# Optimization experiments

Hardware: AMD Instinct MI355X
Metric: run time of the kernel (lower is better)

## Reference

```python
import jax, jax.numpy as jnp
import numpy as np

OH, OW = 32, 32          # adaptive pool output size
NUM_KERNELS = 2
LATENT = 100             # latent_dims = [100, 100]
S = (OH // 2) * (OW // 2)  # in_spatial = 256


def adaptive_avg_pool(x, oh, ow):
    # exact-divisor adaptive avg pool == block mean
    B, C, H, W = x.shape
    return x.reshape(B, C, oh, H // oh, ow, W // ow).mean(axis=(3, 5))


def setup_inputs() -> dict:
    key = jax.random.key(0)
    k1, k2, k3, k4 = jax.random.split(key, 4)
    x = jax.random.normal(k1, (8, 512, 128, 128), dtype=jnp.float32)
    scale = 1.0 / np.sqrt(S)
    psi_w = jax.random.normal(k2, (NUM_KERNELS, S, LATENT), dtype=jnp.float32) * scale  # visible->latent proj
    phi_w = jax.random.normal(k3, (NUM_KERNELS, S, LATENT), dtype=jnp.float32) * scale  # latent->visible proj
    out_w = jax.random.normal(k4, (S, S), dtype=jnp.float32) * scale                    # output linear over spatial feats
    return {"x": x, "psi_w": psi_w, "phi_w": phi_w, "out_w": out_w}


def reference(x, psi_w, phi_w, out_w):
    B, C, H, W = x.shape
    # GAP: adaptive average pool to (OH, OW)
    xg = adaptive_avg_pool(x, OH, OW)                                   # [B,C,32,32]
    # internal 2x2 avg pool (accounts for in_spatial = h/2 * ceil(w/2))
    v = xg.reshape(B, C, OH // 2, 2, OW // 2, 2).mean(axis=(3, 5))
    v = v.reshape(B, C, S)                                              # channel nodes [B,C,S]
    # visible -> latent affinity (softmax over visible/channel nodes)
    A_v2l = jax.nn.softmax(jnp.einsum('bcs,ksd->bkdc', v, psi_w), axis=-1)  # [B,K,d1,C]
    z = jnp.einsum('bkdc,bcs->bkds', A_v2l, v).reshape(B, NUM_KERNELS * LATENT, S)  # [B,Kd1,S]
    # latent -> latent propagation on normalized features
    zn = z / (jnp.linalg.norm(z, axis=-1, keepdims=True) + 1e-6)
    G = jax.nn.softmax(jnp.einsum('bms,bns->bmn', zn, zn), axis=-1)     # [B,Kd1,Kd1]
    zp = jnp.einsum('bmn,bns->bms', G, z).reshape(B, NUM_KERNELS, LATENT, S)
    # latent -> visible affinity (softmax over latent nodes)
    A_l2v = jax.nn.softmax(jnp.einsum('bcs,ksd->bkcd', v, phi_w), axis=-1)  # [B,K,C,d2]
    out = jnp.einsum('bkcd,bkds->bcs', A_l2v, zp)                       # [B,C,S]
    out = jnp.einsum('bcs,st->bct', out, out_w)
    f = v + out                                                          # residual
    attn = jax.nn.sigmoid(f.mean(axis=-1))                               # [B,C]
    return attn[:, :, None, None]                                        # [B,C,1,1]
```

## Files before the change

kernel.cpp:

```cpp
#include <hip/hip_runtime.h>
#include <math.h>

constexpr int Bn = 8, Cn = 512, Sn = 256, Mn = 200, Ln = 100;

constexpr size_t OFF_V    = 0;
constexpr size_t OFF_A    = OFF_V   + (size_t)Bn*Cn*Sn;
constexpr size_t OFF_Z    = OFF_A   + (size_t)Bn*Mn*Cn;
constexpr size_t OFF_INV  = OFF_Z   + (size_t)Bn*Mn*Sn;
constexpr size_t OFF_ZW   = OFF_INV + (size_t)Bn*Mn;
constexpr size_t OFF_ZPW  = OFF_ZW  + (size_t)Bn*Mn;
constexpr size_t OFF_WSUM = OFF_ZPW + (size_t)Bn*Mn;

__device__ __forceinline__ float blk_max(float x, float* red) {
  #pragma unroll
  for (int o = 32; o; o >>= 1) x = fmaxf(x, __shfl_xor(x, o));
  __syncthreads();
  if ((threadIdx.x & 63) == 0) red[threadIdx.x >> 6] = x;
  __syncthreads();
  return fmaxf(fmaxf(red[0], red[1]), fmaxf(red[2], red[3]));
}
__device__ __forceinline__ float blk_sum(float x, float* red) {
  #pragma unroll
  for (int o = 32; o; o >>= 1) x += __shfl_xor(x, o);
  __syncthreads();
  if ((threadIdx.x & 63) == 0) red[threadIdx.x >> 6] = x;
  __syncthreads();
  return red[0] + red[1] + red[2] + red[3];
}

__global__ void k_wsum(const float* __restrict__ w, float* __restrict__ ws) {
  int t = threadIdx.x;
  const float* row = w + (size_t)t * Sn;
  float s = 0.f;
  for (int j = 0; j < Sn; j += 4) {
    float4 f = *(const float4*)(row + j);
    s += f.x + f.y + f.z + f.w;
  }
  ws[OFF_WSUM + t] = s;
}

__global__ void __launch_bounds__(256) k_pool(const float* __restrict__ x,
                                              float* __restrict__ ws) {
  int bc = blockIdx.x;
  const float* plane = x + (size_t)bc * 16384;
  int t = threadIdx.x;
  float part[16];
  #pragma unroll
  for (int i = 0; i < 16; ++i) {
    float4 f = *(const float4*)(plane + i * 1024 + t * 4);
    part[i] = f.x + f.y + f.z + f.w;
  }
  __shared__ float lds[256][17];
  #pragma unroll
  for (int i = 0; i < 16; ++i) lds[t][i] = part[i];
  __syncthreads();
  int i = t >> 4, jj = t & 15;
  float s = 0.f;
  #pragma unroll
  for (int r = 0; r < 8; ++r)
    s += lds[32 * r + 2 * jj][i] + lds[32 * r + 2 * jj + 1][i];
  ws[OFF_V + (size_t)bc * 256 + t] = s * (1.0f / 64.0f);
}

__global__ void __launch_bounds__(256) k_psm(const float* __restrict__ psi,
                                             float* __restrict__ ws) {
  int b = blockIdx.y, g = blockIdx.x, t = threadIdx.x;
  int m0 = g * 8;
  __shared__ float pc[8][256];
  __shared__ float red[4];
  const float* v = ws + OFF_V + (size_t)b * Cn * Sn;
  #pragma unroll
  for (int mm = 0; mm < 8; ++mm) {
    int m = m0 + mm, k = m / Ln, d = m % Ln;
    pc[mm][t] = psi[(size_t)k * Sn * Ln + (size_t)t * Ln + d];
  }
  __syncthreads();
  float acc[2][8];
  #pragma unroll
  for (int ci = 0; ci < 2; ++ci) {
    const float* vp = v + (size_t)(t + ci * 256) * Sn;
    float a[8] = {0, 0, 0, 0, 0, 0, 0, 0};
    for (int s = 0; s < Sn; s += 4) {
      float4 vv = *(const float4*)(vp + s);
      #pragma unroll
      for (int mm = 0; mm < 8; ++mm)
        a[mm] += vv.x * pc[mm][s] + vv.y * pc[mm][s + 1] +
                 vv.z * pc[mm][s + 2] + vv.w * pc[mm][s + 3];
    }
    #pragma unroll
    for (int mm = 0; mm < 8; ++mm) acc[ci][mm] = a[mm];
  }
  #pragma unroll
  for (int mm = 0; mm < 8; ++mm) {
    float mx = blk_max(fmaxf(acc[0][mm], acc[1][mm]), red);
    float e0 = expf(acc[0][mm] - mx), e1 = expf(acc[1][mm] - mx);
    float inv = 1.0f / blk_sum(e0 + e1, red);
    float* Arow = ws + OFF_A + ((size_t)b * Mn + m0 + mm) * Cn;
    Arow[t] = e0 * inv;
    Arow[t + 256] = e1 * inv;
  }
}

__global__ void __launch_bounds__(256) k_z(float* __restrict__ ws) {
  int b = blockIdx.y, g = blockIdx.x, t = threadIdx.x;
  int m0 = g * 8;
  __shared__ float As[8][512];
  __shared__ float red[4];
  const float* v = ws + OFF_V + (size_t)b * Cn * Sn;
  const float* A = ws + OFF_A + (size_t)b * Mn * Cn;
  #pragma unroll
  for (int mm = 0; mm < 8; ++mm) {
    As[mm][t]       = A[(size_t)(m0 + mm) * Cn + t];
    As[mm][t + 256] = A[(size_t)(m0 + mm) * Cn + t + 256];
  }
  __syncthreads();
  float acc[8] = {0, 0, 0, 0, 0, 0, 0, 0};
  for (int c = 0; c < Cn; ++c) {
    float vv = v[(size_t)c * Sn + t];
    #pragma unroll
    for (int mm = 0; mm < 8; ++mm) acc[mm] += As[mm][c] * vv;
  }
  float wsv = ws[OFF_WSUM + t];
  #pragma unroll
  for (int mm = 0; mm < 8; ++mm) {
    int m = m0 + mm;
    ws[OFF_Z + ((size_t)b * Mn + m) * Sn + t] = acc[mm];
    float n2 = blk_sum(acc[mm] * acc[mm], red);
    float zw = blk_sum(acc[mm] * wsv, red);
    if (t == 0) {
      ws[OFF_INV + (size_t)b * Mn + m] = 1.0f / (sqrtf(n2) + 1e-6f);
      ws[OFF_ZW  + (size_t)b * Mn + m] = zw;
    }
  }
}

__global__ void __launch_bounds__(256) k_g(float* __restrict__ ws) {
  int b = blockIdx.y, g = blockIdx.x, t = threadIdx.x;
  int m0 = g * 8;
  __shared__ float zl[8][256];
  __shared__ float invl[200], zwl[200];
  __shared__ float red[4];
  const float* z = ws + OFF_Z + (size_t)b * Mn * Sn;
  #pragma unroll
  for (int mm = 0; mm < 8; ++mm) zl[mm][t] = z[(size_t)(m0 + mm) * Sn + t];
  if (t < Mn) {
    invl[t] = ws[OFF_INV + (size_t)b * Mn + t];
    zwl[t]  = ws[OFF_ZW  + (size_t)b * Mn + t];
  }
  __syncthreads();
  float dot[8] = {0, 0, 0, 0, 0, 0, 0, 0};
  if (t < Mn) {
    const float* zr = z + (size_t)t * Sn;
    for (int s = 0; s < Sn; s += 4) {
      float4 zz = *(const float4*)(zr + s);
      #pragma unroll
      for (int mm = 0; mm < 8; ++mm)
        dot[mm] += zz.x * zl[mm][s] + zz.y * zl[mm][s + 1] +
                   zz.z * zl[mm][s + 2] + zz.w * zl[mm][s + 3];
    }
  }
  #pragma unroll
  for (int mm = 0; mm < 8; ++mm) {
    int m = m0 + mm;
    float val = (t < Mn) ? dot[mm] * invl[m] * invl[t] : -1e30f;
    float mx = blk_max(val, red);
    float e  = (t < Mn) ? expf(val - mx) : 0.f;
    float se  = blk_sum(e, red);
    float sez = blk_sum(e * ((t < Mn) ? zwl[t] : 0.f), red);
    if (t == 0) ws[OFF_ZPW + (size_t)b * Mn + m] = sez / se;
  }
}

__global__ void __launch_bounds__(256) k_out(const float* __restrict__ phi,
                                             float* __restrict__ out,
                                             float* __restrict__ ws) {
  int b = blockIdx.y, cg = blockIdx.x, t = threadIdx.x;
  int c0 = cg * 8;
  __shared__ float vl[8][256];
  __shared__ float zpl[200];
  __shared__ float t2l[16][104];
  __shared__ float resl[2][8];
  __shared__ float vsl[8];
  const float* v = ws + OFF_V + ((size_t)b * Cn + c0) * Sn;
  #pragma unroll
  for (int cc = 0; cc < 8; ++cc) vl[cc][t] = v[(size_t)cc * Sn + t];
  if (t < Mn) zpl[t] = ws[OFF_ZPW + (size_t)b * Mn + t];
  __syncthreads();
  int k = t >> 7, d = t & 127;
  int dd = d < Ln ? d : Ln - 1;
  const float* pp = phi + (size_t)k * Sn * Ln + dd;
  float acc[8] = {0, 0, 0, 0, 0, 0, 0, 0};
  for (int s = 0; s < Sn; ++s) {
    float p = pp[(size_t)s * Ln];
    #pragma unroll
    for (int cc = 0; cc < 8; ++cc) acc[cc] += vl[cc][s] * p;
  }
  if (d < Ln) {
    #pragma unroll
    for (int cc = 0; cc < 8; ++cc) t2l[k * 8 + cc][d] = acc[cc];
  }
  __syncthreads();
  int gg = t >> 4, l = t & 15;
  int k2 = gg >> 3, cc2 = gg & 7;
  float mx = -1e30f;
  for (int dq = l; dq < Ln; dq += 16) mx = fmaxf(mx, t2l[gg][dq]);
  #pragma unroll
  for (int o = 8; o; o >>= 1) mx = fmaxf(mx, __shfl_xor(mx, o));
  float se = 0.f, sez = 0.f;
  for (int dq = l; dq < Ln; dq += 16) {
    float e = expf(t2l[gg][dq] - mx);
    se += e;
    sez += e * zpl[k2 * Ln + dq];
  }
  #pragma unroll
  for (int o = 8; o; o >>= 1) { se += __shfl_xor(se, o); sez += __shfl_xor(sez, o); }
  float vs = 0.f;
  if (k2 == 0) {
    for (int i2 = 0; i2 < 16; ++i2) vs += vl[cc2][i2 * 16 + l];
    #pragma unroll
    for (int o = 8; o; o >>= 1) vs += __shfl_xor(vs, o);
    if (l == 0) vsl[cc2] = vs;
  }
  if (l == 0) resl[k2][cc2] = sez / se;
  __syncthreads();
  if (t < 8) {
    float f = (vsl[t] + resl[0][t] + resl[1][t]) * (1.0f / 256.0f);
    out[(size_t)b * Cn + c0 + t] = 1.0f / (1.0f + expf(-f));
  }
}

extern "C" void kernel_launch(void* const* d_in, const int* in_sizes, int n_in,
                              void* d_out, int out_size, void* d_ws, size_t ws_size,
                              hipStream_t stream) {
  const float* x   = (const float*)d_in[0];
  const float* psi = (const float*)d_in[1];
  const float* phi = (const float*)d_in[2];
  const float* ow  = (const float*)d_in[3];
  float* out = (float*)d_out;
  float* ws  = (float*)d_ws;

  hipLaunchKernelGGL(k_wsum, dim3(1),       dim3(256), 0, stream, ow, ws);
  hipLaunchKernelGGL(k_pool, dim3(4096),    dim3(256), 0, stream, x, ws);
  hipLaunchKernelGGL(k_psm,  dim3(25, 8),   dim3(256), 0, stream, psi, ws);
  hipLaunchKernelGGL(k_z,    dim3(25, 8),   dim3(256), 0, stream, ws);
  hipLaunchKernelGGL(k_g,    dim3(25, 8),   dim3(256), 0, stream, ws);
  hipLaunchKernelGGL(k_out,  dim3(64, 8),   dim3(256), 0, stream, phi, out, ws);
}
```

Before: 156.8 us.

## Fuse softmax-affinity and z kernels, fold wsum into pool, batch block reductions

Merges the psi softmax kernel and the z projection kernel into one 512-thread kernel that keeps the affinity matrix in LDS instead of writing and re-reading it through global memory. Folds the out_w row-sum into an extra block of the pool kernel, which removes a launch. Block reductions now handle four values at once to cut barrier count. k_g is split into 4-row groups to double its grid, and the inner loops use float4 LDS reads. The cost is higher LDS use per block and fewer, larger blocks in the fused kernel.

```diff
diff --git a/kernel.cpp b/kernel.cpp
--- a/kernel.cpp
+++ b/kernel.cpp
@@ -4,46 +4,66 @@
 constexpr int Bn = 8, Cn = 512, Sn = 256, Mn = 200, Ln = 100;
 
 constexpr size_t OFF_V    = 0;
-constexpr size_t OFF_A    = OFF_V   + (size_t)Bn*Cn*Sn;
-constexpr size_t OFF_Z    = OFF_A   + (size_t)Bn*Mn*Cn;
+constexpr size_t OFF_Z    = OFF_V   + (size_t)Bn*Cn*Sn;
 constexpr size_t OFF_INV  = OFF_Z   + (size_t)Bn*Mn*Sn;
 constexpr size_t OFF_ZW   = OFF_INV + (size_t)Bn*Mn;
 constexpr size_t OFF_ZPW  = OFF_ZW  + (size_t)Bn*Mn;
 constexpr size_t OFF_WSUM = OFF_ZPW + (size_t)Bn*Mn;
 
-__device__ __forceinline__ float blk_max(float x, float* red) {
-  #pragma unroll
-  for (int o = 32; o; o >>= 1) x = fmaxf(x, __shfl_xor(x, o));
+template<int NW>
+__device__ __forceinline__ float4 blk_max_f4(float4 x, float4* red) {
+  #pragma unroll
+  for (int o = 32; o; o >>= 1) {
+    x.x = fmaxf(x.x, __shfl_xor(x.x, o));
+    x.y = fmaxf(x.y, __shfl_xor(x.y, o));
+    x.z = fmaxf(x.z, __shfl_xor(x.z, o));
+    x.w = fmaxf(x.w, __shfl_xor(x.w, o));
+  }
   __syncthreads();
   if ((threadIdx.x & 63) == 0) red[threadIdx.x >> 6] = x;
   __syncthreads();
-  return fmaxf(fmaxf(red[0], red[1]), fmaxf(red[2], red[3]));
-}
-__device__ __forceinline__ float blk_sum(float x, float* red) {
-  #pragma unroll
-  for (int o = 32; o; o >>= 1) x += __shfl_xor(x, o);
+  float4 r = red[0];
+  #pragma unroll
+  for (int w = 1; w < NW; ++w) {
+    r.x = fmaxf(r.x, red[w].x); r.y = fmaxf(r.y, red[w].y);
+    r.z = fmaxf(r.z, red[w].z); r.w = fmaxf(r.w, red[w].w);
+  }
+  return r;
+}
+template<int NW>
+__device__ __forceinline__ float4 blk_sum_f4(float4 x, float4* red) {
+  #pragma unroll
+  for (int o = 32; o; o >>= 1) {
+    x.x += __shfl_xor(x.x, o); x.y += __shfl_xor(x.y, o);
+    x.z += __shfl_xor(x.z, o); x.w += __shfl_xor(x.w, o);
+  }
   __syncthreads();
   if ((threadIdx.x & 63) == 0) red[threadIdx.x >> 6] = x;
   __syncthreads();
-  return red[0] + red[1] + red[2] + red[3];
-}
-
-__global__ void k_wsum(const float* __restrict__ w, float* __restrict__ ws) {
+  float4 r = red[0];
+  #pragma unroll
+  for (int w = 1; w < NW; ++w) {
+    r.x += red[w].x; r.y += red[w].y; r.z += red[w].z; r.w += red[w].w;
+  }
+  return r;
+}
+
+__global__ void __launch_bounds__(256) k_pool(const float* __restrict__ x,
+                                              const float* __restrict__ ow,
+                                              float* __restrict__ ws) {
   int t = threadIdx.x;
-  const float* row = w + (size_t)t * Sn;
-  float s = 0.f;
-  for (int j = 0; j < Sn; j += 4) {
-    float4 f = *(const float4*)(row + j);
-    s += f.x + f.y + f.z + f.w;
-  }
-  ws[OFF_WSUM + t] = s;
-}
-
-__global__ void __launch_bounds__(256) k_pool(const float* __restrict__ x,
-                                              float* __restrict__ ws) {
+  if (blockIdx.x == 4096) {
+    const float* row = ow + (size_t)t * Sn;
+    float s = 0.f;
+    for (int j = 0; j < Sn; j += 4) {
+      float4 f = *(const float4*)(row + j);
+      s += f.x + f.y + f.z + f.w;
+    }
+    ws[OFF_WSUM + t] = s;
+    return;
+  }
   int bc = blockIdx.x;
   const float* plane = x + (size_t)bc * 16384;
-  int t = threadIdx.x;
   float part[16];
   #pragma unroll
   for (int i = 0; i < 16; ++i) {
@@ -62,112 +82,142 @@
   ws[OFF_V + (size_t)bc * 256 + t] = s * (1.0f / 64.0f);
 }
 
-__global__ void __launch_bounds__(256) k_psm(const float* __restrict__ psi,
+__global__ void __launch_bounds__(512) k_psz(const float* __restrict__ psi,
                                              float* __restrict__ ws) {
   int b = blockIdx.y, g = blockIdx.x, t = threadIdx.x;
   int m0 = g * 8;
-  __shared__ float pc[8][256];
-  __shared__ float red[4];
+  __shared__ __align__(16) float pc[8][256];
+  __shared__ __align__(16) float As[8][512];
+  __shared__ __align__(16) float zpart[2][8][256];
+  __shared__ float4 red4[8];
   const float* v = ws + OFF_V + (size_t)b * Cn * Sn;
-  #pragma unroll
-  for (int mm = 0; mm < 8; ++mm) {
+
+  for (int e = t; e < 8 * 256; e += 512) {
+    int mm = e >> 8, s = e & 255;
     int m = m0 + mm, k = m / Ln, d = m % Ln;
-    pc[mm][t] = psi[(size_t)k * Sn * Ln + (size_t)t * Ln + d];
-  }
-  __syncthreads();
-  float acc[2][8];
-  #pragma unroll
-  for (int ci = 0; ci < 2; ++ci) {
-    const float* vp = v + (size_t)(t + ci * 256) * Sn;
-    float a[8] = {0, 0, 0, 0, 0, 0, 0, 0};
+    pc[mm][s] = psi[(size_t)k * Sn * Ln + (size_t)s * Ln + d];
+  }
+  __syncthreads();
+
+  float acc[8] = {0, 0, 0, 0, 0, 0, 0, 0};
+  {
+    const float* vp = v + (size_t)t * Sn;
     for (int s = 0; s < Sn; s += 4) {
       float4 vv = *(const float4*)(vp + s);
       #pragma unroll
-      for (int mm = 0; mm < 8; ++mm)
-        a[mm] += vv.x * pc[mm][s] + vv.y * pc[mm][s + 1] +
-                 vv.z * pc[mm][s + 2] + vv.w * pc[mm][s + 3];
-    }
-    #pragma unroll
-    for (int mm = 0; mm < 8; ++mm) acc[ci][mm] = a[mm];
-  }
-  #pragma unroll
-  for (int mm = 0; mm < 8; ++mm) {
-    float mx = blk_max(fmaxf(acc[0][mm], acc[1][mm]), red);
-    float e0 = expf(acc[0][mm] - mx), e1 = expf(acc[1][mm] - mx);
-    float inv = 1.0f / blk_sum(e0 + e1, red);
-    float* Arow = ws + OFF_A + ((size_t)b * Mn + m0 + mm) * Cn;
-    Arow[t] = e0 * inv;
-    Arow[t + 256] = e1 * inv;
-  }
-}
-
-__global__ void __launch_bounds__(256) k_z(float* __restrict__ ws) {
-  int b = blockIdx.y, g = blockIdx.x, t = threadIdx.x;
-  int m0 = g * 8;
-  __shared__ float As[8][512];
-  __shared__ float red[4];
-  const float* v = ws + OFF_V + (size_t)b * Cn * Sn;
-  const float* A = ws + OFF_A + (size_t)b * Mn * Cn;
-  #pragma unroll
-  for (int mm = 0; mm < 8; ++mm) {
-    As[mm][t]       = A[(size_t)(m0 + mm) * Cn + t];
-    As[mm][t + 256] = A[(size_t)(m0 + mm) * Cn + t + 256];
-  }
-  __syncthreads();
-  float acc[8] = {0, 0, 0, 0, 0, 0, 0, 0};
-  for (int c = 0; c < Cn; ++c) {
-    float vv = v[(size_t)c * Sn + t];
-    #pragma unroll
-    for (int mm = 0; mm < 8; ++mm) acc[mm] += As[mm][c] * vv;
-  }
-  float wsv = ws[OFF_WSUM + t];
-  #pragma unroll
-  for (int mm = 0; mm < 8; ++mm) {
-    int m = m0 + mm;
-    ws[OFF_Z + ((size_t)b * Mn + m) * Sn + t] = acc[mm];
-    float n2 = blk_sum(acc[mm] * acc[mm], red);
-    float zw = blk_sum(acc[mm] * wsv, red);
+      for (int mm = 0; mm < 8; ++mm) {
+        float4 p = *(const float4*)&pc[mm][s];
+        acc[mm] += vv.x * p.x + vv.y * p.y + vv.z * p.z + vv.w * p.w;
+      }
+    }
+  }
+  #pragma unroll
+  for (int q = 0; q < 2; ++q) {
+    float4 a = make_float4(acc[4*q], acc[4*q+1], acc[4*q+2], acc[4*q+3]);
+    float4 mx = blk_max_f4<8>(a, red4);
+    float4 e;
+    e.x = expf(a.x - mx.x); e.y = expf(a.y - mx.y);
+    e.z = expf(a.z - mx.z); e.w = expf(a.w - mx.w);
+    float4 se = blk_sum_f4<8>(e, red4);
+    As[4*q+0][t] = e.x / se.x;
+    As[4*q+1][t] = e.y / se.y;
+    As[4*q+2][t] = e.z / se.z;
+    As[4*q+3][t] = e.w / se.w;
+  }
+  __syncthreads();
+
+  int h = t >> 8, s2 = t & 255;
+  float a2[8] = {0, 0, 0, 0, 0, 0, 0, 0};
+  const float* vb = v + (size_t)h * 256 * Sn;
+  for (int c = 0; c < 256; c += 4) {
+    float v0 = vb[(size_t)(c + 0) * Sn + s2];
+    float v1 = vb[(size_t)(c + 1) * Sn + s2];
+    float v2 = vb[(size_t)(c + 2) * Sn + s2];
+    float v3 = vb[(size_t)(c + 3) * Sn + s2];
+    #pragma unroll
+    for (int mm = 0; mm < 8; ++mm) {
+      float4 aa = *(const float4*)&As[mm][h * 256 + c];
+      a2[mm] += aa.x * v0 + aa.y * v1 + aa.z * v2 + aa.w * v3;
+    }
+  }
+  #pragma unroll
+  for (int mm = 0; mm < 8; ++mm) zpart[h][mm][s2] = a2[mm];
+  __syncthreads();
+
+  float zv[8] = {0, 0, 0, 0, 0, 0, 0, 0};
+  float wsv = 0.f;
+  if (t < 256) {
+    wsv = ws[OFF_WSUM + t];
+    float* zo = ws + OFF_Z + ((size_t)b * Mn + m0) * Sn;
+    #pragma unroll
+    for (int mm = 0; mm < 8; ++mm) {
+      zv[mm] = zpart[0][mm][t] + zpart[1][mm][t];
+      zo[(size_t)mm * Sn + t] = zv[mm];
+    }
+  }
+  #pragma unroll
+  for (int q = 0; q < 2; ++q) {
+    float4 sq = make_float4(zv[4*q]*zv[4*q], zv[4*q+1]*zv[4*q+1],
+                            zv[4*q+2]*zv[4*q+2], zv[4*q+3]*zv[4*q+3]);
+    float4 n2 = blk_sum_f4<8>(sq, red4);
+    float4 zw = blk_sum_f4<8>(make_float4(zv[4*q]*wsv, zv[4*q+1]*wsv,
+                                          zv[4*q+2]*wsv, zv[4*q+3]*wsv), red4);
     if (t == 0) {
-      ws[OFF_INV + (size_t)b * Mn + m] = 1.0f / (sqrtf(n2) + 1e-6f);
-      ws[OFF_ZW  + (size_t)b * Mn + m] = zw;
+      float* inv = ws + OFF_INV + (size_t)b * Mn + m0 + 4*q;
+      float* zwp = ws + OFF_ZW  + (size_t)b * Mn + m0 + 4*q;
+      inv[0] = 1.0f / (sqrtf(n2.x) + 1e-6f); zwp[0] = zw.x;
+      inv[1] = 1.0f / (sqrtf(n2.y) + 1e-6f); zwp[1] = zw.y;
+      inv[2] = 1.0f / (sqrtf(n2.z) + 1e-6f); zwp[2] = zw.z;
+      inv[3] = 1.0f / (sqrtf(n2.w) + 1e-6f); zwp[3] = zw.w;
     }
   }
 }
 
 __global__ void __launch_bounds__(256) k_g(float* __restrict__ ws) {
   int b = blockIdx.y, g = blockIdx.x, t = threadIdx.x;
-  int m0 = g * 8;
-  __shared__ float zl[8][256];
+  int m0 = g * 4;
+  __shared__ __align__(16) float zl[4][256];
   __shared__ float invl[200], zwl[200];
-  __shared__ float red[4];
+  __shared__ float4 red4[4];
   const float* z = ws + OFF_Z + (size_t)b * Mn * Sn;
   #pragma unroll
-  for (int mm = 0; mm < 8; ++mm) zl[mm][t] = z[(size_t)(m0 + mm) * Sn + t];
+  for (int mm = 0; mm < 4; ++mm) zl[mm][t] = z[(size_t)(m0 + mm) * Sn + t];
   if (t < Mn) {
     invl[t] = ws[OFF_INV + (size_t)b * Mn + t];
     zwl[t]  = ws[OFF_ZW  + (size_t)b * Mn + t];
   }
   __syncthreads();
-  float dot[8] = {0, 0, 0, 0, 0, 0, 0, 0};
-  if (t < Mn) {
+  bool act = t < Mn;
+  float dot[4] = {0, 0, 0, 0};
+  if (act) {
     const float* zr = z + (size_t)t * Sn;
     for (int s = 0; s < Sn; s += 4) {
       float4 zz = *(const float4*)(zr + s);
       #pragma unroll
-      for (int mm = 0; mm < 8; ++mm)
-        dot[mm] += zz.x * zl[mm][s] + zz.y * zl[mm][s + 1] +
-                   zz.z * zl[mm][s + 2] + zz.w * zl[mm][s + 3];
-    }
-  }
-  #pragma unroll
-  for (int mm = 0; mm < 8; ++mm) {
-    int m = m0 + mm;
-    float val = (t < Mn) ? dot[mm] * invl[m] * invl[t] : -1e30f;
-    float mx = blk_max(val, red);
-    float e  = (t < Mn) ? expf(val - mx) : 0.f;
-    float se  = blk_sum(e, red);
-    float sez = blk_sum(e * ((t < Mn) ? zwl[t] : 0.f), red);
-    if (t == 0) ws[OFF_ZPW + (size_t)b * Mn + m] = sez / se;
+      for (int mm = 0; mm < 4; ++mm) {
+        float4 zl4 = *(const float4*)&zl[mm][s];
+        dot[mm] += zz.x * zl4.x + zz.y * zl4.y + zz.z * zl4.z + zz.w * zl4.w;
+      }
+    }
+  }
+  float4 val;
+  val.x = act ? dot[0] * invl[m0 + 0] * invl[t] : -1e30f;
+  val.y = act ? dot[1] * invl[m0 + 1] * invl[t] : -1e30f;
+  val.z = act ? dot[2] * invl[m0 + 2] * invl[t] : -1e30f;
+  val.w = act ? dot[3] * invl[m0 + 3] * invl[t] : -1e30f;
+  float4 mx = blk_max_f4<4>(val, red4);
+  float4 e;
+  e.x = act ? expf(val.x - mx.x) : 0.f;
+  e.y = act ? expf(val.y - mx.y) : 0.f;
+  e.z = act ? expf(val.z - mx.z) : 0.f;
+  e.w = act ? expf(val.w - mx.w) : 0.f;
+  float4 se = blk_sum_f4<4>(e, red4);
+  float zwn = act ? zwl[t] : 0.f;
+  float4 sez = blk_sum_f4<4>(make_float4(e.x*zwn, e.y*zwn, e.z*zwn, e.w*zwn), red4);
+  if (t == 0) {
+    float* zp = ws + OFF_ZPW + (size_t)b * Mn + m0;
+    zp[0] = sez.x / se.x; zp[1] = sez.y / se.y;
+    zp[2] = sez.z / se.z; zp[3] = sez.w / se.w;
   }
 }
 
@@ -176,7 +226,7 @@
                                              float* __restrict__ ws) {
   int b = blockIdx.y, cg = blockIdx.x, t = threadIdx.x;
   int c0 = cg * 8;
-  __shared__ float vl[8][256];
+  __shared__ __align__(16) float vl[8][256];
   __shared__ float zpl[200];
   __shared__ float t2l[16][104];
   __shared__ float resl[2][8];
@@ -190,10 +240,16 @@
   int dd = d < Ln ? d : Ln - 1;
   const float* pp = phi + (size_t)k * Sn * Ln + dd;
   float acc[8] = {0, 0, 0, 0, 0, 0, 0, 0};
-  for (int s = 0; s < Sn; ++s) {
-    float p = pp[(size_t)s * Ln];
-    #pragma unroll
-    for (int cc = 0; cc < 8; ++cc) acc[cc] += vl[cc][s] * p;
+  for (int s = 0; s < Sn; s += 4) {
+    float p0 = pp[(size_t)(s + 0) * Ln];
+    float p1 = pp[(size_t)(s + 1) * Ln];
+    float p2 = pp[(size_t)(s + 2) * Ln];
+    float p3 = pp[(size_t)(s + 3) * Ln];
+    #pragma unroll
+    for (int cc = 0; cc < 8; ++cc) {
+      float4 vv = *(const float4*)&vl[cc][s];
+      acc[cc] += vv.x * p0 + vv.y * p1 + vv.z * p2 + vv.w * p3;
+    }
   }
   if (d < Ln) {
     #pragma unroll
@@ -239,10 +295,8 @@
   float* out = (float*)d_out;
   float* ws  = (float*)d_ws;
 
-  hipLaunchKernelGGL(k_wsum, dim3(1),       dim3(256), 0, stream, ow, ws);
-  hipLaunchKernelGGL(k_pool, dim3(4096),    dim3(256), 0, stream, x, ws);
-  hipLaunchKernelGGL(k_psm,  dim3(25, 8),   dim3(256), 0, stream, psi, ws);
-  hipLaunchKernelGGL(k_z,    dim3(25, 8),   dim3(256), 0, stream, ws);
-  hipLaunchKernelGGL(k_g,    dim3(25, 8),   dim3(256), 0, stream, ws);
-  hipLaunchKernelGGL(k_out,  dim3(64, 8),   dim3(256), 0, stream, phi, out, ws);
-}
+  hipLaunchKernelGGL(k_pool, dim3(4097),   dim3(256), 0, stream, x, ow, ws);
+  hipLaunchKernelGGL(k_psz,  dim3(25, 8),  dim3(512), 0, stream, psi, ws);
+  hipLaunchKernelGGL(k_g,    dim3(50, 8),  dim3(256), 0, stream, ws);
+  hipLaunchKernelGGL(k_out,  dim3(64, 8),  dim3(256), 0, stream, phi, out, ws);
+}
```

New measurement: 125.8 us. 1.25x faster.
